# Optimization experiments

Measured on AMD Instinct MI355X. Metric: run time of the kernel, lower is better.

The kernel has to match this reference:

```python
import jax, jax.numpy as jnp
import numpy as np

EMB_DIM = 128
NUM_CLS = 128
H = W = 512
K = 131072


def setup_inputs() -> dict:
    key = jax.random.key(0)
    k1, k2, k3, k4 = jax.random.split(key, 4)
    gc_features = jax.random.normal(k1, (1, EMB_DIM, H, W), dtype=jnp.float32)
    cls_id_map = jax.random.randint(k2, (1, K), 0, H * W, dtype=jnp.int64)
    # nn.Linear(emb_dim, num_cls) params, kaiming-uniform-ish scale
    lim = 1.0 / np.sqrt(EMB_DIM)
    W_cls = jax.random.uniform(k3, (NUM_CLS, EMB_DIM), dtype=jnp.float32, minval=-lim, maxval=lim)
    b_cls = jax.random.uniform(k4, (NUM_CLS,), dtype=jnp.float32, minval=-lim, maxval=lim)
    return {"gc_features": gc_features, "cls_id_map": cls_id_map, "W_cls": W_cls, "b_cls": b_cls}


def reference(gc_features, cls_id_map, W_cls, b_cls):
    B, C, h, w = gc_features.shape
    # _tranpose_and_gather_feat: [B,C,H,W] -> [B,HW,C], gather rows by inds
    feat = gc_features.reshape(B, C, h * w).transpose(0, 2, 1)      # [B, HW, C]
    feat = jnp.take_along_axis(feat, cls_id_map[:, :, None], axis=1)  # [B, K, C]
    feat = feat[0]                                                   # squeeze(0) -> [K, C]
    pred = feat @ W_cls.T + b_cls                                    # [K, num_cls]
    return jax.nn.softmax(pred, axis=1)
```

## Files before the change

### kernel.cpp

```cpp
#include <hip/hip_runtime.h>
#include <hip/hip_bf16.h>
#include <hip/hip_fp16.h>

#define HW      262144
#define NCH     128
#define NCLS    128
#define KROWS   131072
#define NTILE   4096
#define CAP     192

typedef short  bf16x8 __attribute__((ext_vector_type(8)));
typedef float  f32x4  __attribute__((ext_vector_type(4)));

__device__ inline ushort f2bf(float f) {
    union { float f; unsigned u; } v; v.f = f;
    unsigned u = v.u;
    unsigned r = (u + 0x7FFFu + ((u >> 16) & 1u)) >> 16;
    return (ushort)r;
}

__global__ __launch_bounds__(256) void prep(const float* __restrict__ Wc,
                                            ushort* __restrict__ Wf,
                                            int4* __restrict__ cnt4) {
    if (blockIdx.x < 64) {
        int e    = blockIdx.x * 256 + threadIdx.x;
        int j    = e & 7;
        int slot = e >> 3;
        int lane = slot & 63;
        int kk   = (slot >> 6) & 3;
        int nt   = slot >> 8;
        int n = (nt << 4) + (lane & 15);
        int k = (kk << 5) + ((lane >> 4) << 3) + j;
        Wf[e] = f2bf(Wc[n * NCH + k]);
    } else {
        cnt4[(blockIdx.x - 64) * 256 + threadIdx.x] = make_int4(0, 0, 0, 0);
    }
}

__global__ __launch_bounds__(256) void csr_fill(const int* __restrict__ idx,
                                                int* __restrict__ cnt,
                                                int* __restrict__ pairs) {
    int k = blockIdx.x * 256 + threadIdx.x;
    int p = idx[k];
    int tile = p >> 6;
    int pos = atomicAdd(&cnt[tile], 1);
    if (pos < CAP) pairs[tile * CAP + pos] = (k << 6) | (p & 63);
}

__global__ __launch_bounds__(256) void gemm_scatter(const float* __restrict__ gc,
                                                    const ushort* __restrict__ Wf,
                                                    const float* __restrict__ bias,
                                                    const int* __restrict__ cnt,
                                                    const int* __restrict__ pairs,
                                                    float* __restrict__ out) {
    __shared__ ushort Wl[NCLS * NCH];
    __shared__ ushort AO[64 * NCH];

    const int t    = threadIdx.x;
    const int lane = t & 63;
    const int wv   = t >> 6;
    const int l15  = lane & 15;
    const int quad = lane >> 4;
    const int m0   = blockIdx.x << 6;

    float4 va[8];
    #pragma unroll
    for (int i = 0; i < 4; ++i) {
        int q  = (i << 8) + t;
        int cp = q >> 4, mq = q & 15;
        int c0 = cp << 1, m = mq << 2;
        va[2 * i]     = *(const float4*)&gc[(size_t)c0 * HW + m0 + m];
        va[2 * i + 1] = *(const float4*)&gc[(size_t)(c0 + 1) * HW + m0 + m];
    }

    #pragma unroll
    for (int i = 0; i < 8; ++i) {
        const ushort* g = Wf + (i << 11) + (t << 3);
        ushort*       l = Wl + (i << 11) + (t << 3);
        __builtin_amdgcn_global_load_lds(
            (const __attribute__((address_space(1))) unsigned*)g,
            (__attribute__((address_space(3))) unsigned*)l, 16, 0, 0);
    }

    float bcol[8];
    #pragma unroll
    for (int nt = 0; nt < 8; ++nt) bcol[nt] = bias[(nt << 4) + l15];

    #pragma unroll
    for (int i = 0; i < 4; ++i) {
        int q  = (i << 8) + t;
        int cp = q >> 4, mq = q & 15;
        int c0 = cp << 1, m = mq << 2;
        int kk = c0 >> 5, kc2 = (c0 >> 3) & 3, j = c0 & 7;
        const float* a0 = (const float*)&va[2 * i];
        const float* a1 = (const float*)&va[2 * i + 1];
        #pragma unroll
        for (int d = 0; d < 4; ++d) {
            int row  = m + d;
            int slot = ((((row >> 4) << 2) + kk) << 6) + (row & 15) + (kc2 << 4);
            slot ^= (row >> 2) & 7;
            __hip_bfloat162 pk = __float22bfloat162_rn(make_float2(a0[d], a1[d]));
            *(ushort2*)&AO[(slot << 3) + j] = *(ushort2*)&pk;
        }
    }
    __syncthreads();

    f32x4 acc[8];
    #pragma unroll
    for (int i = 0; i < 8; ++i) acc[i] = (f32x4){0.f, 0.f, 0.f, 0.f};

    #pragma unroll
    for (int kk = 0; kk < 4; ++kk) {
        int aslot = ((((wv << 2) + kk) << 6) + lane) ^ ((((wv << 4) + l15) >> 2) & 7);
        bf16x8 a = *(const bf16x8*)&AO[aslot << 3];
        #pragma unroll
        for (int nt = 0; nt < 8; ++nt) {
            bf16x8 b = *(const bf16x8*)&Wl[((((nt << 2) + kk) << 6) + lane) << 3];
            acc[nt] = __builtin_amdgcn_mfma_f32_16x16x32_bf16(a, b, acc[nt], 0, 0, 0);
        }
    }

    float inv[4];
    #pragma unroll
    for (int rr = 0; rr < 4; ++rr) {
        float s = 0.f;
        #pragma unroll
        for (int nt = 0; nt < 8; ++nt) {
            acc[nt][rr] = __expf(acc[nt][rr] + bcol[nt]);
            s += acc[nt][rr];
        }
        s += __shfl_xor(s, 1, 64);
        s += __shfl_xor(s, 2, 64);
        s += __shfl_xor(s, 4, 64);
        s += __shfl_xor(s, 8, 64);
        inv[rr] = 1.0f / s;
    }

    const int g = ((quad & 1) << 2) | (quad & 2);
    #pragma unroll
    for (int nt = 0; nt < 8; ++nt) {
        int cl = ((nt << 1) + (l15 >> 3)) ^ g;
        #pragma unroll
        for (int rr = 0; rr < 4; ++rr) {
            int row = (wv << 4) + (quad << 2) + rr;
            AO[(row << 7) + (cl << 3) + (l15 & 7)] =
                __half_as_ushort(__float2half_rn(acc[nt][rr] * inv[rr]));
        }
    }
    __syncthreads();

    const int nb = min(cnt[blockIdx.x], CAP);
    const int* pb = pairs + blockIdx.x * CAP;
    #pragma unroll 2
    for (int e = wv; e < nb; e += 4) {
        int pk  = pb[e];
        int row = pk & 63;
        int k   = pk >> 6;
        int qd  = (row >> 2) & 3;
        int gq  = ((qd & 1) << 2) | (qd & 2);
        int cl  = (lane >> 2) ^ gq;
        __half2 h = *(const __half2*)&AO[(row << 7) + (cl << 3) + ((lane << 1) & 7)];
        float2 f = __half22float2(h);
        *(float2*)&out[((size_t)k << 7) + (lane << 1)] = f;
    }
}

extern "C" void kernel_launch(void* const* d_in, const int* in_sizes, int n_in,
                              void* d_out, int out_size, void* d_ws, size_t ws_size,
                              hipStream_t stream) {
    const float* gc   = (const float*)d_in[0];
    const int*   idx  = (const int*)d_in[1];
    const float* Wc   = (const float*)d_in[2];
    const float* bias = (const float*)d_in[3];
    float* out = (float*)d_out;

    char* ws = (char*)d_ws;
    int*    cnt   = (int*)(ws);
    int*    pairs = (int*)(ws + 0x10000);
    ushort* Wf    = (ushort*)(ws + 0x400000);

    prep        <<<dim3(68),       dim3(256), 0, stream>>>(Wc, Wf, (int4*)cnt);
    csr_fill    <<<dim3(KROWS/256),dim3(256), 0, stream>>>(idx, cnt, pairs);
    gemm_scatter<<<dim3(NTILE),    dim3(256), 0, stream>>>(gc, Wf, bias, cnt, pairs, out);
}
```

Before: 236.2 us.

## Make each wave own a 16-row bucket and drop LDS staging of weights

```diff
diff --git a/kernel.cpp b/kernel.cpp
--- a/kernel.cpp
+++ b/kernel.cpp
@@ -6,8 +6,8 @@
 #define NCH     128
 #define NCLS    128
 #define KROWS   131072
-#define NTILE   4096
-#define CAP     192
+#define NBKT    16384
+#define CAP     48
 
 typedef short  bf16x8 __attribute__((ext_vector_type(8)));
 typedef float  f32x4  __attribute__((ext_vector_type(4)));
@@ -42,19 +42,18 @@
                                                 int* __restrict__ pairs) {
     int k = blockIdx.x * 256 + threadIdx.x;
     int p = idx[k];
-    int tile = p >> 6;
-    int pos = atomicAdd(&cnt[tile], 1);
-    if (pos < CAP) pairs[tile * CAP + pos] = (k << 6) | (p & 63);
+    int b = p >> 4;
+    int pos = atomicAdd(&cnt[b], 1);
+    if (pos < CAP) pairs[b * CAP + pos] = (k << 4) | (p & 15);
 }
 
-__global__ __launch_bounds__(256) void gemm_scatter(const float* __restrict__ gc,
-                                                    const ushort* __restrict__ Wf,
-                                                    const float* __restrict__ bias,
-                                                    const int* __restrict__ cnt,
-                                                    const int* __restrict__ pairs,
-                                                    float* __restrict__ out) {
-    __shared__ ushort Wl[NCLS * NCH];
-    __shared__ ushort AO[64 * NCH];
+__global__ __launch_bounds__(256, 4) void gemm_scatter(const float* __restrict__ gc,
+                                                       const ushort* __restrict__ Wf,
+                                                       const float* __restrict__ bias,
+                                                       const int* __restrict__ cnt,
+                                                       const int* __restrict__ pairs,
+                                                       float* __restrict__ out) {
+    __shared__ ushort AO[64 * NCLS];
 
     const int t    = threadIdx.x;
     const int lane = t & 63;
@@ -62,48 +61,37 @@
     const int l15  = lane & 15;
     const int quad = lane >> 4;
     const int m0   = blockIdx.x << 6;
+    const int mw   = m0 + (wv << 4) + l15;
 
-    float4 va[8];
+    const int bkt = (blockIdx.x << 2) + wv;
+    int nb = cnt[bkt];
+    int pkr = 0;
+    if (lane < CAP) pkr = pairs[bkt * CAP + lane];
+
+    float a_raw[32];
     #pragma unroll
-    for (int i = 0; i < 4; ++i) {
-        int q  = (i << 8) + t;
-        int cp = q >> 4, mq = q & 15;
-        int c0 = cp << 1, m = mq << 2;
-        va[2 * i]     = *(const float4*)&gc[(size_t)c0 * HW + m0 + m];
-        va[2 * i + 1] = *(const float4*)&gc[(size_t)(c0 + 1) * HW + m0 + m];
-    }
+    for (int kk = 0; kk < 4; ++kk)
+        #pragma unroll
+        for (int j = 0; j < 8; ++j)
+            a_raw[(kk << 3) + j] =
+                gc[(size_t)((kk << 5) + (quad << 3) + j) * HW + mw];
 
+    bf16x8 b0[8];
     #pragma unroll
-    for (int i = 0; i < 8; ++i) {
-        const ushort* g = Wf + (i << 11) + (t << 3);
-        ushort*       l = Wl + (i << 11) + (t << 3);
-        __builtin_amdgcn_global_load_lds(
-            (const __attribute__((address_space(1))) unsigned*)g,
-            (__attribute__((address_space(3))) unsigned*)l, 16, 0, 0);
-    }
+    for (int nt = 0; nt < 8; ++nt)
+        b0[nt] = *(const bf16x8*)&Wf[((((nt << 2) + 0) << 6) + lane) << 3];
 
-    float bcol[8];
+    bf16x8 afr[4];
     #pragma unroll
-    for (int nt = 0; nt < 8; ++nt) bcol[nt] = bias[(nt << 4) + l15];
-
-    #pragma unroll
-    for (int i = 0; i < 4; ++i) {
-        int q  = (i << 8) + t;
-        int cp = q >> 4, mq = q & 15;
-        int c0 = cp << 1, m = mq << 2;
-        int kk = c0 >> 5, kc2 = (c0 >> 3) & 3, j = c0 & 7;
-        const float* a0 = (const float*)&va[2 * i];
-        const float* a1 = (const float*)&va[2 * i + 1];
+    for (int kk = 0; kk < 4; ++kk) {
+        ushort2* ap = (ushort2*)&afr[kk];
         #pragma unroll
-        for (int d = 0; d < 4; ++d) {
-            int row  = m + d;
-            int slot = ((((row >> 4) << 2) + kk) << 6) + (row & 15) + (kc2 << 4);
-            slot ^= (row >> 2) & 7;
-            __hip_bfloat162 pk = __float22bfloat162_rn(make_float2(a0[d], a1[d]));
-            *(ushort2*)&AO[(slot << 3) + j] = *(ushort2*)&pk;
+        for (int jj = 0; jj < 4; ++jj) {
+            __hip_bfloat162 pk = __float22bfloat162_rn(
+                make_float2(a_raw[(kk << 3) + 2 * jj], a_raw[(kk << 3) + 2 * jj + 1]));
+            ap[jj] = *(ushort2*)&pk;
         }
     }
-    __syncthreads();
 
     f32x4 acc[8];
     #pragma unroll
@@ -111,14 +99,22 @@
 
     #pragma unroll
     for (int kk = 0; kk < 4; ++kk) {
-        int aslot = ((((wv << 2) + kk) << 6) + lane) ^ ((((wv << 4) + l15) >> 2) & 7);
-        bf16x8 a = *(const bf16x8*)&AO[aslot << 3];
+        bf16x8 bn[8];
+        if (kk < 3) {
+            #pragma unroll
+            for (int nt = 0; nt < 8; ++nt)
+                bn[nt] = *(const bf16x8*)&Wf[((((nt << 2) + kk + 1) << 6) + lane) << 3];
+        }
         #pragma unroll
-        for (int nt = 0; nt < 8; ++nt) {
-            bf16x8 b = *(const bf16x8*)&Wl[((((nt << 2) + kk) << 6) + lane) << 3];
-            acc[nt] = __builtin_amdgcn_mfma_f32_16x16x32_bf16(a, b, acc[nt], 0, 0, 0);
-        }
+        for (int nt = 0; nt < 8; ++nt)
+            acc[nt] = __builtin_amdgcn_mfma_f32_16x16x32_bf16(afr[kk], b0[nt], acc[nt], 0, 0, 0);
+        #pragma unroll
+        for (int nt = 0; nt < 8; ++nt) b0[nt] = bn[nt];
     }
+
+    float bcol[8];
+    #pragma unroll
+    for (int nt = 0; nt < 8; ++nt) bcol[nt] = bias[(nt << 4) + l15];
 
     float inv[4];
     #pragma unroll
@@ -147,19 +143,16 @@
                 __half_as_ushort(__float2half_rn(acc[nt][rr] * inv[rr]));
         }
     }
-    __syncthreads();
 
-    const int nb = min(cnt[blockIdx.x], CAP);
-    const int* pb = pairs + blockIdx.x * CAP;
-    #pragma unroll 2
-    for (int e = wv; e < nb; e += 4) {
-        int pk  = pb[e];
-        int row = pk & 63;
-        int k   = pk >> 6;
-        int qd  = (row >> 2) & 3;
+    nb = min(nb, CAP);
+    for (int i = 0; i < nb; ++i) {
+        int pk  = __shfl(pkr, i, 64);
+        int row = pk & 15;
+        int k   = pk >> 4;
+        int qd  = row >> 2;
         int gq  = ((qd & 1) << 2) | (qd & 2);
         int cl  = (lane >> 2) ^ gq;
-        __half2 h = *(const __half2*)&AO[(row << 7) + (cl << 3) + ((lane << 1) & 7)];
+        __half2 h = *(const __half2*)&AO[(((wv << 4) + row) << 7) + (cl << 3) + ((lane << 1) & 7)];
         float2 f = __half22float2(h);
         *(float2*)&out[((size_t)k << 7) + (lane << 1)] = f;
     }
@@ -179,7 +172,7 @@
     int*    pairs = (int*)(ws + 0x10000);
     ushort* Wf    = (ushort*)(ws + 0x400000);
 
-    prep        <<<dim3(68),       dim3(256), 0, stream>>>(Wc, Wf, (int4*)cnt);
-    csr_fill    <<<dim3(KROWS/256),dim3(256), 0, stream>>>(idx, cnt, pairs);
-    gemm_scatter<<<dim3(NTILE),    dim3(256), 0, stream>>>(gc, Wf, bias, cnt, pairs, out);
+    prep        <<<dim3(80),        dim3(256), 0, stream>>>(Wc, Wf, (int4*)cnt);
+    csr_fill    <<<dim3(KROWS/256), dim3(256), 0, stream>>>(idx, cnt, pairs);
+    gemm_scatter<<<dim3(HW/64),     dim3(256), 0, stream>>>(gc, Wf, bias, cnt, pairs, out);
 }
```

Result: slower. 268.8 us (+13.8%).
